# Kernel optimization log

Hardware: AMD Instinct MI355X
Metric: run time of the kernel (lower is better)

## Reference

```python
import jax, jax.numpy as jnp
import numpy as np

N, E, B = 50000, 600000, 64
C_IN, H, C_OUT, L = 128, 128, 64, 3
BN_EPS = 1e-5


def setup_inputs() -> dict:
    key = jax.random.key(0)
    ks = iter(jax.random.split(key, 40))

    def w(shape, fan_in):
        return jax.random.normal(next(ks), shape, jnp.float32) / np.sqrt(fan_in).astype(np.float32)

    return {
        "x": jax.random.normal(next(ks), (N, C_IN), jnp.float32),
        "edge_index": jax.random.randint(next(ks), (2, E), 0, N),
        "batch": jnp.sort(jax.random.randint(next(ks), (N,), 0, B)),
        # GINConv MLPs: Linear(in,h) -> BN -> ReLU -> Linear(h,h)   (stacked over L; C_IN == H)
        "convW1": w((L, C_IN, H), C_IN), "convb1": jnp.zeros((L, H), jnp.float32),
        "bn_g": jnp.ones((L, H), jnp.float32), "bn_b": jnp.zeros((L, H), jnp.float32),
        "convW2": w((L, H, H), H), "convb2": jnp.zeros((L, H), jnp.float32),
        # reconstruction head: Linear(h,h)-ReLU-Linear(h,h)-ReLU-Linear(h,4)-ReLU
        "recW1": w((H, H), H), "recb1": jnp.zeros((H,), jnp.float32),
        "recW2": w((H, H), H), "recb2": jnp.zeros((H,), jnp.float32),
        "recW3": w((H, 4), H), "recb3": jnp.zeros((4,), jnp.float32),
        # final MLP([h,h,out], norm=None): Linear(h,h)-ReLU-(dropout, eval=identity)-Linear(h,out)
        "mlpW1": w((H, H), H), "mlpb1": jnp.zeros((H,), jnp.float32),
        "mlpW2": w((H, C_OUT), H), "mlpb2": jnp.zeros((C_OUT,), jnp.float32),
    }


def reference(x, edge_index, batch, convW1, convb1, bn_g, bn_b, convW2, convb2,
              recW1, recb1, recW2, recb2, recW3, recb3, mlpW1, mlpb1, mlpW2, mlpb2):
    src, dst = edge_index[0], edge_index[1]
    for l in range(L):
        # GIN aggregation: out_i = nn((1+eps)*x_i + sum_{j->i} x_j), eps = 0
        agg = jax.ops.segment_sum(x[src], dst, num_segments=N)  # [N, d]
        h = (x + agg) @ convW1[l] + convb1[l]                   # [N, H]
        mu = h.mean(axis=0)
        var = jnp.var(h, axis=0)                                # biased, torch BN train mode
        h = bn_g[l] * (h - mu) * jax.lax.rsqrt(var + BN_EPS) + bn_b[l]
        h = jax.nn.relu(h) @ convW2[l] + convb2[l]
        x = jax.nn.relu(h)                                      # outer .relu() in forward
    # reconstruction branch on node features
    x_rec = jax.nn.relu(x @ recW1 + recb1)
    x_rec = jax.nn.relu(x_rec @ recW2 + recb2)
    x_rec = jax.nn.relu(x_rec @ recW3 + recb3)                  # [N, 4]
    # global_add_pool keyed by graph id
    pooled = jax.ops.segment_sum(x, batch, num_segments=B)      # [B, H]
    out = jax.nn.relu(pooled @ mlpW1 + mlpb1) @ mlpW2 + mlpb2   # [B, C_OUT]
    return (out, x_rec)
```

## Files before the change

kernel.cpp:

```cpp
#include <hip/hip_runtime.h>

#define NN 50000
#define EE 600000
#define BB 64
#define CH 128
#define LL 3
#define NGB 391
#define NGA 3128
#define NSB 196
#define NPB 392

typedef unsigned short u16;
typedef unsigned int u32;
typedef short s16x8 __attribute__((ext_vector_type(8)));
typedef float f32x4 __attribute__((ext_vector_type(4)));


__device__ __forceinline__ u16 f2b(float f) {
    u32 x = __float_as_uint(f);
    return (u16)((x + 0x7FFFu + ((x >> 16) & 1u)) >> 16);
}
__device__ __forceinline__ float b2f(u16 u) {
    return __uint_as_float(((u32)u) << 16);
}

__global__ __launch_bounds__(256) void k_prep(
    const float* __restrict__ x, u16* __restrict__ x16,
    const float* __restrict__ cW1, const float* __restrict__ cW2,
    const float* __restrict__ rW1, const float* __restrict__ rW2,
    const float* __restrict__ rW3, u16* __restrict__ Wt,
    int* __restrict__ deg, float* __restrict__ pooled,
    float* __restrict__ gstats) {
    int gid = blockIdx.x * 256 + threadIdx.x;

    long base = (long)gid * 8;
    if (base < (long)NN * CH) {
        float4 f0 = *(const float4*)(x + base);
        float4 f1 = *(const float4*)(x + base + 4);
        union { u16 pk[8]; uint4 v; } uu;
        uu.pk[0] = f2b(f0.x); uu.pk[1] = f2b(f0.y);
        uu.pk[2] = f2b(f0.z); uu.pk[3] = f2b(f0.w);
        uu.pk[4] = f2b(f1.x); uu.pk[5] = f2b(f1.y);
        uu.pk[6] = f2b(f1.z); uu.pk[7] = f2b(f1.w);
        long row = base >> 7;
        int col = (int)(base & 127);
        *(uint4*)(x16 + ((size_t)(col >> 5) * NN + row) * 32 + (col & 31)) = uu.v;
    }
    if (gid < 8 * 16384) {
        int slot = gid >> 14;
        int wi = gid & 16383;
        int k = wi >> 7, n = wi & 127;
        const float* src = slot < 3 ? cW1 + slot * 16384
                         : slot < 6 ? cW2 + (slot - 3) * 16384
                         : slot == 6 ? rW1 : rW2;
        Wt[slot * 16384 + n * 128 + k] = f2b(src[wi]);
    } else if (gid < 9 * 16384) {
        int j = gid - 8 * 16384;
        int n = j >> 7, k = j & 127;
        Wt[8 * 16384 + j] = (n < 4) ? f2b(rW3[k * 4 + n]) : (u16)0;
    }
    if (gid < NN) deg[gid] = 0;
    int j2 = gid - NN;
    if (j2 >= 0 && j2 < BB * CH) pooled[j2] = 0.f;
    int k2 = j2 - BB * CH;
    if (k2 >= 0 && k2 < 3 * 256) gstats[k2] = 0.f;
}

__global__ __launch_bounds__(256) void k_count(const int* __restrict__ ei,
                                               int* __restrict__ deg) {
    int e = blockIdx.x * 256 + threadIdx.x;
    if (e < EE) atomicAdd(&deg[ei[EE + e]], 1);
}

__global__ __launch_bounds__(256) void k_scanA(const int* __restrict__ deg,
                                               int* __restrict__ bsum) {
    __shared__ int sm[256];
    int i = blockIdx.x * 256 + threadIdx.x;
    sm[threadIdx.x] = (i < NN) ? deg[i] : 0;
    __syncthreads();
    for (int off = 128; off > 0; off >>= 1) {
        if (threadIdx.x < off) sm[threadIdx.x] += sm[threadIdx.x + off];
        __syncthreads();
    }
    if (threadIdx.x == 0) bsum[blockIdx.x] = sm[0];
}

__global__ __launch_bounds__(256) void k_scanB(const int* __restrict__ deg,
                                               const int* __restrict__ bsum,
                                               int* __restrict__ rowptr,
                                               int* __restrict__ cur) {
    __shared__ int sb[256], sd[256];
    int t = threadIdx.x;
    sb[t] = (t < NSB) ? bsum[t] : 0;
    __syncthreads();
    for (int off = 1; off < 256; off <<= 1) {
        int v = (t >= off) ? sb[t - off] : 0;
        __syncthreads();
        sb[t] += v;
        __syncthreads();
    }
    int blockOff = (blockIdx.x == 0) ? 0 : sb[blockIdx.x - 1];
    int i = blockIdx.x * 256 + t;
    int d = (i < NN) ? deg[i] : 0;
    sd[t] = d;
    __syncthreads();
    for (int off = 1; off < 256; off <<= 1) {
        int v = (t >= off) ? sd[t - off] : 0;
        __syncthreads();
        sd[t] += v;
        __syncthreads();
    }
    int excl = blockOff + sd[t] - d;
    if (i < NN) { rowptr[i] = excl; cur[i] = excl; }
    if (i == NN - 1) rowptr[NN] = excl + d;
}

__global__ __launch_bounds__(256) void k_fill(const int* __restrict__ ei,
                                              int* __restrict__ cur,
                                              u16* __restrict__ perm) {
    int e = blockIdx.x * 256 + threadIdx.x;
    if (e < EE) {
        int dst = ei[EE + e];
        int idx = atomicAdd(&cur[dst], 1);
        perm[idx] = (u16)ei[e];
    }
}

__global__ __launch_bounds__(256) void k_gather(const u16* __restrict__ x,
                                                const int* __restrict__ rowptr,
                                                const u16* __restrict__ perm,
                                                u16* __restrict__ y) {
    int chunk = blockIdx.x & 3;
    int rb = blockIdx.x >> 2;
    int dst = rb * 64 + (threadIdx.x >> 2);
    if (dst >= NN) return;
    int gl = threadIdx.x & 3;
    const u16* xb = x + (size_t)chunk * NN * 32 + gl * 8;
    int beg = rowptr[dst], end = rowptr[dst + 1];
    union { u16 pk[8]; uint4 v; } uu;
    uu.v = *(const uint4*)(xb + (size_t)dst * 32);
    float a[8], b[8], c[8], d[8];
#pragma unroll
    for (int j = 0; j < 8; ++j) { a[j] = b2f(uu.pk[j]); b[j] = 0.f; c[j] = 0.f; d[j] = 0.f; }
    int e = beg;
    for (; e + 3 < end; e += 4) {
        int s0 = perm[e], s1 = perm[e + 1], s2 = perm[e + 2], s3 = perm[e + 3];
        union { u16 pk[8]; uint4 v; } v0, v1, v2, v3;
        v0.v = *(const uint4*)(xb + (size_t)s0 * 32);
        v1.v = *(const uint4*)(xb + (size_t)s1 * 32);
        v2.v = *(const uint4*)(xb + (size_t)s2 * 32);
        v3.v = *(const uint4*)(xb + (size_t)s3 * 32);
#pragma unroll
        for (int j = 0; j < 8; ++j) {
            a[j] += b2f(v0.pk[j]); b[j] += b2f(v1.pk[j]);
            c[j] += b2f(v2.pk[j]); d[j] += b2f(v3.pk[j]);
        }
    }
    for (; e < end; ++e) {
        int s0 = perm[e];
        union { u16 pk[8]; uint4 v; } v0;
        v0.v = *(const uint4*)(xb + (size_t)s0 * 32);
#pragma unroll
        for (int j = 0; j < 8; ++j) a[j] += b2f(v0.pk[j]);
    }
    union { u16 pk[8]; uint4 v; } ov;
#pragma unroll
    for (int j = 0; j < 8; ++j) ov.pk[j] = f2b((a[j] + b[j]) + (c[j] + d[j]));
    *(uint4*)(y + (size_t)chunk * NN * 32 + (size_t)dst * 32 + gl * 8) = ov.v;
}

__device__ __forceinline__ void stageB8(const u16* __restrict__ Wt, u16* sB,
                                        int s, int rr) {
#pragma unroll
    for (int it = 0; it < 8; ++it) {
        int n = it * 16 + rr;
        uint4 u = *(const uint4*)(Wt + n * CH + 8 * s);
        *(uint4*)(&sB[n * CH + ((s ^ (n & 15)) * 8)]) = u;
    }
}

__device__ __forceinline__ void mfma8(const u16* sA, const u16* sB,
                                      f32x4 acc[2][8], int wv, int quad, int l16) {
    f32x4 z = {0.f, 0.f, 0.f, 0.f};
#pragma unroll
    for (int m = 0; m < 2; ++m)
#pragma unroll
        for (int t = 0; t < 8; ++t) acc[m][t] = z;
    const u16* pa0 = sA + (wv * 32 + l16) * CH;
    const u16* pa1 = pa0 + 16 * CH;
#pragma unroll
    for (int kc = 0; kc < 4; ++kc) {
        int off = (((kc << 2) | quad) ^ l16) << 3;
        s16x8 a0 = *(const s16x8*)(pa0 + off);
        s16x8 a1 = *(const s16x8*)(pa1 + off);
#pragma unroll
        for (int t = 0; t < 8; ++t) {
            s16x8 bfr = *(const s16x8*)(sB + (t * 16 + l16) * CH + off);
            acc[0][t] = __builtin_amdgcn_mfma_f32_16x16x32_bf16(a0, bfr, acc[0][t], 0, 0, 0);
            acc[1][t] = __builtin_amdgcn_mfma_f32_16x16x32_bf16(a1, bfr, acc[1][t], 0, 0, 0);
        }
    }
}

__device__ __forceinline__ void biasrelu(f32x4 acc[2][8],
                                         const float* __restrict__ bias, int l16) {
#pragma unroll
    for (int t = 0; t < 8; ++t) {
        float bv = bias[t * 16 + l16];
#pragma unroll
        for (int m = 0; m < 2; ++m)
#pragma unroll
            for (int r = 0; r < 4; ++r)
                acc[m][t][r] = fmaxf(acc[m][t][r] + bv, 0.f);
    }
}

__device__ __forceinline__ void restage(const f32x4 acc[2][8], u16* sA,
                                        int wv, int quad, int l16) {
#pragma unroll
    for (int t = 0; t < 8; ++t) {
        int chunk = (t << 1) | (l16 >> 3);
        int o7 = l16 & 7;
#pragma unroll
        for (int m = 0; m < 2; ++m)
#pragma unroll
            for (int r = 0; r < 4; ++r) {
                int lr = wv * 32 + m * 16 + quad * 4 + r;
                sA[lr * CH + ((chunk ^ (lr & 15)) << 3) + o7] = f2b(acc[m][t][r]);
            }
    }
}

__global__ __launch_bounds__(256, 2) void k_gemm1(
    const u16* __restrict__ y16, const u16* __restrict__ Wt, int layer,
    const float* __restrict__ cb1, float* __restrict__ gstats,
    u16* __restrict__ h16) {
    __shared__ u16 sA[128 * CH];
    __shared__ u16 sB[128 * CH];
    const int tid = threadIdx.x;
    const int s = tid & 15, rr = tid >> 4;
    const int r0 = blockIdx.x * 128;
    const int lane = tid & 63, wv = tid >> 6, quad = lane >> 4, l16 = lane & 15;

    stageB8(Wt + layer * 16384, sB, s, rr);
#pragma unroll
    for (int it = 0; it < 8; ++it) {
        int lr = it * 16 + rr, gr = r0 + lr;
        union { u16 pk[8]; uint4 v; } uu;
        if (gr < NN) {
            uu.v = *(const uint4*)(y16 + ((size_t)(s >> 2) * NN + gr) * 32 + (s & 3) * 8);
        } else {
#pragma unroll
            for (int j = 0; j < 8; ++j) uu.pk[j] = 0;
        }
        *(uint4*)(&sA[lr * CH + ((s ^ (lr & 15)) * 8)]) = uu.v;
    }
    __syncthreads();
    f32x4 acc[2][8];
    mfma8(sA, sB, acc, wv, quad, l16);

    float ss[8], qq[8];
#pragma unroll
    for (int t = 0; t < 8; ++t) {
        float bv = cb1[t * 16 + l16];
        ss[t] = 0.f; qq[t] = 0.f;
#pragma unroll
        for (int m = 0; m < 2; ++m) {
            int rbase = r0 + wv * 32 + m * 16 + quad * 4;
#pragma unroll
            for (int r = 0; r < 4; ++r) {
                float v = acc[m][t][r] + bv;
                acc[m][t][r] = v;
                if (rbase + r < NN) { ss[t] += v; qq[t] += v * v; }
            }
        }
    }
#pragma unroll
    for (int t = 0; t < 8; ++t) {
        ss[t] += __shfl_xor(ss[t], 16);
        ss[t] += __shfl_xor(ss[t], 32);
        qq[t] += __shfl_xor(qq[t], 16);
        qq[t] += __shfl_xor(qq[t], 32);
    }
    float* red = (float*)sA;
    __syncthreads();
    if (lane < 16) {
#pragma unroll
        for (int t = 0; t < 8; ++t) {
            red[wv * 256 + t * 16 + l16] = ss[t];
            red[wv * 256 + 128 + t * 16 + l16] = qq[t];
        }
    }
    __syncthreads();
    unsafeAtomicAdd(&gstats[tid],
                    red[tid] + red[256 + tid] + red[512 + tid] + red[768 + tid]);

#pragma unroll
    for (int t = 0; t < 8; ++t) {
        int col = t * 16 + l16;
#pragma unroll
        for (int m = 0; m < 2; ++m)
#pragma unroll
            for (int r = 0; r < 4; ++r) {
                int row = r0 + wv * 32 + m * 16 + quad * 4 + r;
                if (row < NN) h16[(long)row * CH + col] = f2b(acc[m][t][r]);
            }
    }
}

template <bool LAST>
__global__ __launch_bounds__(256, 2) void k_gemm2(
    const u16* __restrict__ h16, const u16* __restrict__ Wt, int layer,
    const float* __restrict__ g, const float* __restrict__ bbeta,
    const float* __restrict__ gstats, const float* __restrict__ cb2,
    u16* __restrict__ xc,
    const float* __restrict__ rb1, const float* __restrict__ rb2,
    const float* __restrict__ rb3, float* __restrict__ x_rec) {
    __shared__ u16 sA[128 * CH];
    __shared__ u16 sB[128 * CH];
    __shared__ float snorm[256];
    const int tid = threadIdx.x;
    const int s = tid & 15, rr = tid >> 4;
    const int r0 = blockIdx.x * 128;
    const int lane = tid & 63, wv = tid >> 6, quad = lane >> 4, l16 = lane & 15;

    if (tid < 128) {
        float sum = gstats[tid];
        float sq = gstats[128 + tid];
        float mu = sum / (float)NN;
        float var = sq / (float)NN - mu * mu;
        float sc = g[tid] * rsqrtf(var + 1e-5f);
        snorm[tid] = sc;
        snorm[128 + tid] = bbeta[tid] - mu * sc;
    }
    stageB8(Wt + (3 + layer) * 16384, sB, s, rr);
    __syncthreads();

#pragma unroll
    for (int it = 0; it < 8; ++it) {
        int lr = it * 16 + rr, gr = r0 + lr;
        union { u16 pk[8]; uint4 v; } uu;
        if (gr < NN) {
            uu.v = *(const uint4*)(h16 + (long)gr * CH + 8 * s);
#pragma unroll
            for (int j = 0; j < 8; ++j) {
                int c = 8 * s + j;
                float v = fmaxf(b2f(uu.pk[j]) * snorm[c] + snorm[128 + c], 0.f);
                uu.pk[j] = f2b(v);
            }
        } else {
#pragma unroll
            for (int j = 0; j < 8; ++j) uu.pk[j] = 0;
        }
        *(uint4*)(&sA[lr * CH + ((s ^ (lr & 15)) * 8)]) = uu.v;
    }
    __syncthreads();
    f32x4 acc[2][8];
    mfma8(sA, sB, acc, wv, quad, l16);
    biasrelu(acc, cb2, l16);
#pragma unroll
    for (int t = 0; t < 8; ++t) {
        u16* xcp = xc + (size_t)(t >> 1) * NN * 32 + (t & 1) * 16 + l16;
#pragma unroll
        for (int m = 0; m < 2; ++m)
#pragma unroll
            for (int r = 0; r < 4; ++r) {
                int row = r0 + wv * 32 + m * 16 + quad * 4 + r;
                if (row < NN) xcp[(size_t)row * 32] = f2b(acc[m][t][r]);
            }
    }

    if constexpr (LAST) {
        __syncthreads();
        restage(acc, sA, wv, quad, l16);
        stageB8(Wt + 6 * 16384, sB, s, rr);
        __syncthreads();
        mfma8(sA, sB, acc, wv, quad, l16);
        biasrelu(acc, rb1, l16);
        __syncthreads();
        restage(acc, sA, wv, quad, l16);
        stageB8(Wt + 7 * 16384, sB, s, rr);
        __syncthreads();
        mfma8(sA, sB, acc, wv, quad, l16);
        biasrelu(acc, rb2, l16);
        __syncthreads();
        restage(acc, sA, wv, quad, l16);
        {
            int n = rr;
            uint4 u = *(const uint4*)(Wt + 8 * 16384 + n * CH + 8 * s);
            *(uint4*)(&sB[n * CH + ((s ^ (n & 15)) * 8)]) = u;
        }
        __syncthreads();
        f32x4 a4[2];
        a4[0] = (f32x4){0.f, 0.f, 0.f, 0.f};
        a4[1] = (f32x4){0.f, 0.f, 0.f, 0.f};
        const u16* pa0 = sA + (wv * 32 + l16) * CH;
        const u16* pa1 = pa0 + 16 * CH;
#pragma unroll
        for (int kc = 0; kc < 4; ++kc) {
            int off = (((kc << 2) | quad) ^ l16) << 3;
            s16x8 a0 = *(const s16x8*)(pa0 + off);
            s16x8 a1 = *(const s16x8*)(pa1 + off);
            s16x8 bfr = *(const s16x8*)(sB + l16 * CH + off);
            a4[0] = __builtin_amdgcn_mfma_f32_16x16x32_bf16(a0, bfr, a4[0], 0, 0, 0);
            a4[1] = __builtin_amdgcn_mfma_f32_16x16x32_bf16(a1, bfr, a4[1], 0, 0, 0);
        }
        if (l16 < 4) {
            float bv = rb3[l16];
#pragma unroll
            for (int m = 0; m < 2; ++m)
#pragma unroll
                for (int r = 0; r < 4; ++r) {
                    int row = r0 + wv * 32 + m * 16 + quad * 4 + r;
                    if (row < NN) x_rec[(long)row * 4 + l16] = fmaxf(a4[m][r] + bv, 0.f);
                }
        }
    }
}

__global__ __launch_bounds__(256) void k_pool(const u16* __restrict__ x,
                                              const int* __restrict__ batch,
                                              float* __restrict__ pooled) {
    int r0 = blockIdx.x * 128;
    if (r0 >= NN) return;
    int rend = r0 + 128 < NN ? r0 + 128 : NN;
    int c = threadIdx.x & 127;
    int half = threadIdx.x >> 7;
    int r = r0 + half;
    if (r >= rend) return;
    const u16* xp = x + (size_t)(c >> 5) * NN * 32 + (c & 31);
    int g = batch[r];
    float s = 0.f;
    for (; r < rend; r += 2) {
        int gg = batch[r];
        if (gg != g) {
            unsafeAtomicAdd(pooled + g * CH + c, s);
            s = 0.f;
            g = gg;
        }
        s += b2f(xp[(size_t)r * 32]);
    }
    unsafeAtomicAdd(pooled + g * CH + c, s);
}

__global__ __launch_bounds__(128) void k_mlp(const float* __restrict__ pooled,
                                             const float* __restrict__ W1,
                                             const float* __restrict__ b1,
                                             const float* __restrict__ W2,
                                             const float* __restrict__ b2,
                                             float* __restrict__ out) {
    __shared__ float p[128], t1[128];
    int b = blockIdx.x, t = threadIdx.x;
    p[t] = pooled[b * CH + t];
    __syncthreads();
    float acc = b1[t];
    for (int k = 0; k < 128; ++k) acc += p[k] * W1[k * 128 + t];
    t1[t] = fmaxf(acc, 0.f);
    __syncthreads();
    if (t < 64) {
        float o = b2[t];
        for (int k = 0; k < 128; ++k) o += t1[k] * W2[k * 64 + t];
        out[b * 64 + t] = o;
    }
}

extern "C" void kernel_launch(void* const* d_in, const int* in_sizes, int n_in,
                              void* d_out, int out_size, void* d_ws, size_t ws_size,
                              hipStream_t stream) {
    const float* x_in   = (const float*)d_in[0];
    const int*   ei     = (const int*)d_in[1];
    const int*   batch  = (const int*)d_in[2];
    const float* convW1 = (const float*)d_in[3];
    const float* convb1 = (const float*)d_in[4];
    const float* bn_g   = (const float*)d_in[5];
    const float* bn_b   = (const float*)d_in[6];
    const float* convW2 = (const float*)d_in[7];
    const float* convb2 = (const float*)d_in[8];
    const float* recW1  = (const float*)d_in[9];
    const float* recb1  = (const float*)d_in[10];
    const float* recW2  = (const float*)d_in[11];
    const float* recb2  = (const float*)d_in[12];
    const float* recW3  = (const float*)d_in[13];
    const float* recb3  = (const float*)d_in[14];
    const float* mlpW1  = (const float*)d_in[15];
    const float* mlpb1  = (const float*)d_in[16];
    const float* mlpW2  = (const float*)d_in[17];
    const float* mlpb2  = (const float*)d_in[18];

    float* out   = (float*)d_out;
    float* x_rec = out + 4096;

    char* w = (char*)d_ws;
    u16*   x16    = (u16*)w;    w += (size_t)NN * CH * 2;
    u16*   y16    = (u16*)w;    w += (size_t)NN * CH * 2;
    u16*   h16    = (u16*)w;    w += (size_t)NN * CH * 2;
    u16*   xc     = (u16*)w;    w += (size_t)NN * CH * 2;
    u16*   Wt     = (u16*)w;    w += (size_t)9 * 16384 * 2;
    float* gstats = (float*)w;  w += (size_t)3 * 256 * 4;
    float* pooled = (float*)w;  w += (size_t)BB * CH * 4;
    int*   deg    = (int*)w;    w += (size_t)NN * 4;
    int*   bsum   = (int*)w;    w += (size_t)NSB * 4;
    int*   rowptr = (int*)w;    w += (size_t)(NN + 1) * 4;
    int*   cur    = (int*)w;    w += (size_t)NN * 4;
    u16*   perm   = (u16*)w;    w += (size_t)EE * 2;

    dim3 b256(256), b128(128);

    k_prep<<<3125, b256, 0, stream>>>(x_in, x16, convW1, convW2, recW1, recW2,
                                      recW3, Wt, deg, pooled, gstats);
    k_count<<<2344, b256, 0, stream>>>(ei, deg);
    k_scanA<<<NSB, b256, 0, stream>>>(deg, bsum);
    k_scanB<<<NSB, b256, 0, stream>>>(deg, bsum, rowptr, cur);
    k_fill<<<2344, b256, 0, stream>>>(ei, cur, perm);

    const u16* cur_x = x16;
    for (int l = 0; l < LL; ++l) {
        k_gather<<<NGA, b256, 0, stream>>>(cur_x, rowptr, perm, y16);
        k_gemm1<<<NGB, b256, 0, stream>>>(y16, Wt, l, convb1 + l * 128,
                                          gstats + l * 256, h16);
        if (l < LL - 1)
            k_gemm2<false><<<NGB, b256, 0, stream>>>(
                h16, Wt, l, bn_g + l * 128, bn_b + l * 128, gstats + l * 256,
                convb2 + l * 128, xc, recb1, recb2, recb3, x_rec);
        else
            k_gemm2<true><<<NGB, b256, 0, stream>>>(
                h16, Wt, l, bn_g + l * 128, bn_b + l * 128, gstats + l * 256,
                convb2 + l * 128, xc, recb1, recb2, recb3, x_rec);
        cur_x = xc;
    }
    k_pool<<<NPB, b256, 0, stream>>>(xc, batch, pooled);
    k_mlp<<<64, b128, 0, stream>>>(pooled, mlpW1, mlpb1, mlpW2, mlpb2, out);
}
```

Measured before the change: 371.8 us.

## Recompute first GEMM in gemm2 instead of storing h16; degree-sort gather rows

The first GEMM kernel now only accumulates batch-norm statistics and no longer writes the pre-norm activations. The second kernel recomputes y@W1 from the aggregated features, folds bias and BN into a per-column scale and shift, and chains into the second GEMM through shared memory. This trades a 12.8MB write and read per layer for redundant MFMA work. Separately, nodes are bucketed by in-degree with a counting sort so each gather block handles destinations of similar degree, reducing divergence at the cost of extra preprocessing kernels and scattered output writes.

```diff
diff --git a/kernel.cpp b/kernel.cpp
--- a/kernel.cpp
+++ b/kernel.cpp
@@ -30,7 +30,7 @@
     const float* __restrict__ rW1, const float* __restrict__ rW2,
     const float* __restrict__ rW3, u16* __restrict__ Wt,
     int* __restrict__ deg, float* __restrict__ pooled,
-    float* __restrict__ gstats) {
+    float* __restrict__ gstats, int* __restrict__ bcnt) {
     int gid = blockIdx.x * 256 + threadIdx.x;
 
     long base = (long)gid * 8;
@@ -64,6 +64,8 @@
     if (j2 >= 0 && j2 < BB * CH) pooled[j2] = 0.f;
     int k2 = j2 - BB * CH;
     if (k2 >= 0 && k2 < 3 * 256) gstats[k2] = 0.f;
+    int l2 = k2 - 3 * 256;
+    if (l2 >= 0 && l2 < 128) bcnt[l2] = 0;
 }
 
 __global__ __launch_bounds__(256) void k_count(const int* __restrict__ ei,
@@ -73,24 +75,42 @@
 }
 
 __global__ __launch_bounds__(256) void k_scanA(const int* __restrict__ deg,
-                                               int* __restrict__ bsum) {
+                                               int* __restrict__ bsum,
+                                               int* __restrict__ bcnt) {
     __shared__ int sm[256];
-    int i = blockIdx.x * 256 + threadIdx.x;
-    sm[threadIdx.x] = (i < NN) ? deg[i] : 0;
-    __syncthreads();
+    __shared__ int hb[64];
+    int t = threadIdx.x;
+    int i = blockIdx.x * 256 + t;
+    int d = (i < NN) ? deg[i] : -1;
+    sm[t] = (d > 0) ? d : 0;
+    if (t < 64) hb[t] = 0;
+    __syncthreads();
+    if (d >= 0) atomicAdd(&hb[d > 63 ? 63 : d], 1);
     for (int off = 128; off > 0; off >>= 1) {
-        if (threadIdx.x < off) sm[threadIdx.x] += sm[threadIdx.x + off];
-        __syncthreads();
-    }
-    if (threadIdx.x == 0) bsum[blockIdx.x] = sm[0];
+        if (t < off) sm[t] += sm[t + off];
+        __syncthreads();
+    }
+    if (t == 0) bsum[blockIdx.x] = sm[0];
+    if (t < 64 && hb[t]) atomicAdd(&bcnt[t], hb[t]);
 }
 
 __global__ __launch_bounds__(256) void k_scanB(const int* __restrict__ deg,
                                                const int* __restrict__ bsum,
                                                int* __restrict__ rowptr,
-                                               int* __restrict__ cur) {
+                                               int* __restrict__ cur,
+                                               const int* __restrict__ bcnt,
+                                               int* __restrict__ bcur) {
     __shared__ int sb[256], sd[256];
     int t = threadIdx.x;
+    if (blockIdx.x == 0 && t < 64) {
+        int v = bcnt[t];
+        int inc = v;
+        for (int off = 1; off < 64; off <<= 1) {
+            int n = __shfl_up(inc, off);
+            if (t >= off) inc += n;
+        }
+        bcur[t] = inc - v;
+    }
     sb[t] = (t < NSB) ? bsum[t] : 0;
     __syncthreads();
     for (int off = 1; off < 256; off <<= 1) {
@@ -126,14 +146,36 @@
     }
 }
 
+__global__ __launch_bounds__(256) void k_order(const int* __restrict__ deg,
+                                               int* __restrict__ bcur,
+                                               u16* __restrict__ order) {
+    __shared__ int hb[64], base[64];
+    int t = threadIdx.x;
+    int i = blockIdx.x * 256 + t;
+    if (t < 64) hb[t] = 0;
+    __syncthreads();
+    int b = -1, rank = 0;
+    if (i < NN) {
+        int d = deg[i];
+        b = d > 63 ? 63 : d;
+        rank = atomicAdd(&hb[b], 1);
+    }
+    __syncthreads();
+    if (t < 64 && hb[t]) base[t] = atomicAdd(&bcur[t], hb[t]);
+    __syncthreads();
+    if (i < NN) order[base[b] + rank] = (u16)i;
+}
+
 __global__ __launch_bounds__(256) void k_gather(const u16* __restrict__ x,
                                                 const int* __restrict__ rowptr,
                                                 const u16* __restrict__ perm,
+                                                const u16* __restrict__ order,
                                                 u16* __restrict__ y) {
     int chunk = blockIdx.x & 3;
     int rb = blockIdx.x >> 2;
-    int dst = rb * 64 + (threadIdx.x >> 2);
-    if (dst >= NN) return;
+    int idx = rb * 64 + (threadIdx.x >> 2);
+    if (idx >= NN) return;
+    int dst = order[idx];
     int gl = threadIdx.x & 3;
     const u16* xb = x + (size_t)chunk * NN * 32 + gl * 8;
     int beg = rowptr[dst], end = rowptr[dst + 1];
@@ -179,6 +221,22 @@
     }
 }
 
+__device__ __forceinline__ void stageAcm(const u16* __restrict__ f, u16* sA,
+                                         int r0, int s, int rr) {
+#pragma unroll
+    for (int it = 0; it < 8; ++it) {
+        int lr = it * 16 + rr, gr = r0 + lr;
+        union { u16 pk[8]; uint4 v; } uu;
+        if (gr < NN) {
+            uu.v = *(const uint4*)(f + ((size_t)(s >> 2) * NN + gr) * 32 + (s & 3) * 8);
+        } else {
+#pragma unroll
+            for (int j = 0; j < 8; ++j) uu.pk[j] = 0;
+        }
+        *(uint4*)(&sA[lr * CH + ((s ^ (lr & 15)) * 8)]) = uu.v;
+    }
+}
+
 __device__ __forceinline__ void mfma8(const u16* sA, const u16* sB,
                                       f32x4 acc[2][8], int wv, int quad, int l16) {
     f32x4 z = {0.f, 0.f, 0.f, 0.f};
@@ -233,8 +291,7 @@
 
 __global__ __launch_bounds__(256, 2) void k_gemm1(
     const u16* __restrict__ y16, const u16* __restrict__ Wt, int layer,
-    const float* __restrict__ cb1, float* __restrict__ gstats,
-    u16* __restrict__ h16) {
+    const float* __restrict__ cb1, float* __restrict__ gstats) {
     __shared__ u16 sA[128 * CH];
     __shared__ u16 sB[128 * CH];
     const int tid = threadIdx.x;
@@ -243,18 +300,7 @@
     const int lane = tid & 63, wv = tid >> 6, quad = lane >> 4, l16 = lane & 15;
 
     stageB8(Wt + layer * 16384, sB, s, rr);
-#pragma unroll
-    for (int it = 0; it < 8; ++it) {
-        int lr = it * 16 + rr, gr = r0 + lr;
-        union { u16 pk[8]; uint4 v; } uu;
-        if (gr < NN) {
-            uu.v = *(const uint4*)(y16 + ((size_t)(s >> 2) * NN + gr) * 32 + (s & 3) * 8);
-        } else {
-#pragma unroll
-            for (int j = 0; j < 8; ++j) uu.pk[j] = 0;
-        }
-        *(uint4*)(&sA[lr * CH + ((s ^ (lr & 15)) * 8)]) = uu.v;
-    }
+    stageAcm(y16, sA, r0, s, rr);
     __syncthreads();
     f32x4 acc[2][8];
     mfma8(sA, sB, acc, wv, quad, l16);
@@ -270,7 +316,6 @@
 #pragma unroll
             for (int r = 0; r < 4; ++r) {
                 float v = acc[m][t][r] + bv;
-                acc[m][t][r] = v;
                 if (rbase + r < NN) { ss[t] += v; qq[t] += v * v; }
             }
         }
@@ -294,26 +339,14 @@
     __syncthreads();
     unsafeAtomicAdd(&gstats[tid],
                     red[tid] + red[256 + tid] + red[512 + tid] + red[768 + tid]);
-
-#pragma unroll
-    for (int t = 0; t < 8; ++t) {
-        int col = t * 16 + l16;
-#pragma unroll
-        for (int m = 0; m < 2; ++m)
-#pragma unroll
-            for (int r = 0; r < 4; ++r) {
-                int row = r0 + wv * 32 + m * 16 + quad * 4 + r;
-                if (row < NN) h16[(long)row * CH + col] = f2b(acc[m][t][r]);
-            }
-    }
 }
 
 template <bool LAST>
 __global__ __launch_bounds__(256, 2) void k_gemm2(
-    const u16* __restrict__ h16, const u16* __restrict__ Wt, int layer,
+    const u16* __restrict__ y16, const u16* __restrict__ Wt, int layer,
     const float* __restrict__ g, const float* __restrict__ bbeta,
-    const float* __restrict__ gstats, const float* __restrict__ cb2,
-    u16* __restrict__ xc,
+    const float* __restrict__ gstats, const float* __restrict__ cb1,
+    const float* __restrict__ cb2, u16* __restrict__ xc,
     const float* __restrict__ rb1, const float* __restrict__ rb2,
     const float* __restrict__ rb3, float* __restrict__ x_rec) {
     __shared__ u16 sA[128 * CH];
@@ -331,31 +364,28 @@
         float var = sq / (float)NN - mu * mu;
         float sc = g[tid] * rsqrtf(var + 1e-5f);
         snorm[tid] = sc;
-        snorm[128 + tid] = bbeta[tid] - mu * sc;
-    }
+        snorm[128 + tid] = (cb1[tid] - mu) * sc + bbeta[tid];
+    }
+    stageB8(Wt + layer * 16384, sB, s, rr);
+    stageAcm(y16, sA, r0, s, rr);
+    __syncthreads();
+    f32x4 acc[2][8];
+    mfma8(sA, sB, acc, wv, quad, l16);
+
+#pragma unroll
+    for (int t = 0; t < 8; ++t) {
+        int col = t * 16 + l16;
+        float sc = snorm[col], sh = snorm[128 + col];
+#pragma unroll
+        for (int m = 0; m < 2; ++m)
+#pragma unroll
+            for (int r = 0; r < 4; ++r)
+                acc[m][t][r] = fmaxf(acc[m][t][r] * sc + sh, 0.f);
+    }
+    __syncthreads();
+    restage(acc, sA, wv, quad, l16);
     stageB8(Wt + (3 + layer) * 16384, sB, s, rr);
     __syncthreads();
-
-#pragma unroll
-    for (int it = 0; it < 8; ++it) {
-        int lr = it * 16 + rr, gr = r0 + lr;
-        union { u16 pk[8]; uint4 v; } uu;
-        if (gr < NN) {
-            uu.v = *(const uint4*)(h16 + (long)gr * CH + 8 * s);
-#pragma unroll
-            for (int j = 0; j < 8; ++j) {
-                int c = 8 * s + j;
-                float v = fmaxf(b2f(uu.pk[j]) * snorm[c] + snorm[128 + c], 0.f);
-                uu.pk[j] = f2b(v);
-            }
-        } else {
-#pragma unroll
-            for (int j = 0; j < 8; ++j) uu.pk[j] = 0;
-        }
-        *(uint4*)(&sA[lr * CH + ((s ^ (lr & 15)) * 8)]) = uu.v;
-    }
-    __syncthreads();
-    f32x4 acc[2][8];
     mfma8(sA, sB, acc, wv, quad, l16);
     biasrelu(acc, cb2, l16);
 #pragma unroll
@@ -493,7 +523,6 @@
     char* w = (char*)d_ws;
     u16*   x16    = (u16*)w;    w += (size_t)NN * CH * 2;
     u16*   y16    = (u16*)w;    w += (size_t)NN * CH * 2;
-    u16*   h16    = (u16*)w;    w += (size_t)NN * CH * 2;
     u16*   xc     = (u16*)w;    w += (size_t)NN * CH * 2;
     u16*   Wt     = (u16*)w;    w += (size_t)9 * 16384 * 2;
     float* gstats = (float*)w;  w += (size_t)3 * 256 * 4;
@@ -502,30 +531,34 @@
     int*   bsum   = (int*)w;    w += (size_t)NSB * 4;
     int*   rowptr = (int*)w;    w += (size_t)(NN + 1) * 4;
     int*   cur    = (int*)w;    w += (size_t)NN * 4;
+    int*   bcnt   = (int*)w;    w += (size_t)64 * 4;
+    int*   bcur   = (int*)w;    w += (size_t)64 * 4;
     u16*   perm   = (u16*)w;    w += (size_t)EE * 2;
+    u16*   order  = (u16*)w;    w += (size_t)NN * 2;
 
     dim3 b256(256), b128(128);
 
     k_prep<<<3125, b256, 0, stream>>>(x_in, x16, convW1, convW2, recW1, recW2,
-                                      recW3, Wt, deg, pooled, gstats);
+                                      recW3, Wt, deg, pooled, gstats, bcnt);
     k_count<<<2344, b256, 0, stream>>>(ei, deg);
-    k_scanA<<<NSB, b256, 0, stream>>>(deg, bsum);
-    k_scanB<<<NSB, b256, 0, stream>>>(deg, bsum, rowptr, cur);
+    k_scanA<<<NSB, b256, 0, stream>>>(deg, bsum, bcnt);
+    k_scanB<<<NSB, b256, 0, stream>>>(deg, bsum, rowptr, cur, bcnt, bcur);
     k_fill<<<2344, b256, 0, stream>>>(ei, cur, perm);
+    k_order<<<NSB, b256, 0, stream>>>(deg, bcur, order);
 
     const u16* cur_x = x16;
     for (int l = 0; l < LL; ++l) {
-        k_gather<<<NGA, b256, 0, stream>>>(cur_x, rowptr, perm, y16);
+        k_gather<<<NGA, b256, 0, stream>>>(cur_x, rowptr, perm, order, y16);
         k_gemm1<<<NGB, b256, 0, stream>>>(y16, Wt, l, convb1 + l * 128,
-                                          gstats + l * 256, h16);
+                                          gstats + l * 256);
         if (l < LL - 1)
             k_gemm2<false><<<NGB, b256, 0, stream>>>(
-                h16, Wt, l, bn_g + l * 128, bn_b + l * 128, gstats + l * 256,
-                convb2 + l * 128, xc, recb1, recb2, recb3, x_rec);
+                y16, Wt, l, bn_g + l * 128, bn_b + l * 128, gstats + l * 256,
+                convb1 + l * 128, convb2 + l * 128, xc, recb1, recb2, recb3, x_rec);
         else
             k_gemm2<true><<<NGB, b256, 0, stream>>>(
-                h16, Wt, l, bn_g + l * 128, bn_b + l * 128, gstats + l * 256,
-                convb2 + l * 128, xc, recb1, recb2, recb3, x_rec);
+                y16, Wt, l, bn_g + l * 128, bn_b + l * 128, gstats + l * 256,
+                convb1 + l * 128, convb2 + l * 128, xc, recb1, recb2, recb3, x_rec);
         cur_x = xc;
     }
     k_pool<<<NPB, b256, 0, stream>>>(xc, batch, pooled);
```

After: 398.5 us. 7.2% more time.
